# Kernel optimization log

Measured on AMD Instinct MI355X. Metric: run time of the kernel, lower is better.

The kernel has to match this reference:

```python
import jax, jax.numpy as jnp
import numpy as np

B, D, F, S, R = 2048, 1024, 1024, 64, 16


def _lora_dense(x, ids, kernel, bias, la, lb):
    # base: frozen dense path (stop_gradient mirrors the original module)
    base = x @ jax.lax.stop_gradient(kernel)
    if bias is not None:
        base = base + jax.lax.stop_gradient(bias)
    a = la[ids]            # (B, D, R) per-example adapter gather
    b = lb[ids]            # (B, R, F)
    low = jnp.einsum('bd,bdr->br', x, a)
    delta = jnp.einsum('br,brf->bf', low, b)
    return base + delta


def setup_inputs() -> dict:
    key = jax.random.key(0)
    ks = jax.random.split(key, 32)
    i = iter(range(32))
    d = {}
    d['carry'] = jax.random.normal(ks[next(i)], (B, F), jnp.float32)
    d['inputs'] = jax.random.normal(ks[next(i)], (B, D), jnp.float32)
    d['adapter_ids'] = jax.random.randint(ks[next(i)], (B,), 0, S)
    kscale = 1.0 / np.sqrt(D)
    for g in ['ir', 'iu', 'ic']:
        d[f'w_{g}'] = jax.random.normal(ks[next(i)], (D, F), jnp.float32) * kscale
        d[f'bias_{g}'] = jax.random.normal(ks[next(i)], (F,), jnp.float32) * 0.01
        d[f'la_{g}'] = jax.random.normal(ks[next(i)], (S, D, R), jnp.float32) * 0.02
        d[f'lb_{g}'] = jax.random.normal(ks[next(i)], (S, R, F), jnp.float32) * 0.01
    for g in ['rr', 'ru', 'rc']:
        d[f'w_{g}'] = jax.random.normal(ks[next(i)], (F, F), jnp.float32) * kscale
        d[f'la_{g}'] = jax.random.normal(ks[next(i)], (S, F, R), jnp.float32) * 0.02
        d[f'lb_{g}'] = jax.random.normal(ks[next(i)], (S, R, F), jnp.float32) * 0.01
    return d


def reference(carry, inputs, adapter_ids,
              w_ir, bias_ir, la_ir, lb_ir,
              w_iu, bias_iu, la_iu, lb_iu,
              w_ic, bias_ic, la_ic, lb_ic,
              w_rr, la_rr, lb_rr,
              w_ru, la_ru, lb_ru,
              w_rc, la_rc, lb_rc):
    ids = adapter_ids
    reset = jax.nn.sigmoid(
        _lora_dense(inputs, ids, w_ir, bias_ir, la_ir, lb_ir)
        + _lora_dense(carry, ids, w_rr, None, la_rr, lb_rr))
    update = jax.nn.sigmoid(
        _lora_dense(inputs, ids, w_iu, bias_iu, la_iu, lb_iu)
        + _lora_dense(carry, ids, w_ru, None, la_ru, lb_ru))
    candidate = jnp.tanh(
        _lora_dense(inputs, ids, w_ic, bias_ic, la_ic, lb_ic)
        + reset * _lora_dense(carry, ids, w_rc, None, la_rc, lb_rc))
    new_carry = (1.0 - update) * candidate + update * carry
    return new_carry
```

## Files before the change

### kernel.cpp

```cpp
#include <hip/hip_runtime.h>
#include <stdint.h>

#define B_  2048
#define D_  1024
#define F_  1024
#define S_  64
#define R_  16

typedef __attribute__((ext_vector_type(8))) short  s16x8;
typedef __attribute__((ext_vector_type(4))) unsigned short u16x4;
typedef __attribute__((ext_vector_type(8))) unsigned short u16x8;
typedef __attribute__((ext_vector_type(4))) float  f32x4;

__device__ __forceinline__ unsigned short f2b(float f){
  unsigned u = __float_as_uint(f);
  u = u + 0x7fffu + ((u >> 16) & 1u);
  return (unsigned short)(u >> 16);
}
__device__ __forceinline__ float b2f(unsigned short s){
  return __uint_as_float(((unsigned)s) << 16);
}

__device__ __forceinline__ void gload16(const void* g, void* l){
  __builtin_amdgcn_global_load_lds((const __attribute__((address_space(1))) unsigned int*)g,
                                   (__attribute__((address_space(3))) unsigned int*)l, 16, 0, 0);
}

#define W0OFF 0
#define W1OFF 2097152
#define W2OFF 4194304
#define W3OFF 5242880

__global__ __launch_bounds__(256) void prep_kernel(
    const float* __restrict__ x, const float* __restrict__ carry,
    unsigned short* __restrict__ XC,
    const float* __restrict__ w_ir, const float* __restrict__ w_rr,
    const float* __restrict__ w_iu, const float* __restrict__ w_ru,
    const float* __restrict__ w_ic, const float* __restrict__ w_rc,
    unsigned short* __restrict__ Wt_all,
    const int* __restrict__ ids, int* __restrict__ starts, int* __restrict__ order){
  int bx = blockIdx.x;
  int t = threadIdx.x;
  if (bx < 2048){
    int i = bx * 256 + t;
    int b = i >> 8;
    int j = (i & 255) * 4;
    float4 xv = *(const float4*)&x[(size_t)b*D_ + j];
    float4 cv = *(const float4*)&carry[(size_t)b*F_ + j];
    u16x4 xs, cs;
    xs[0]=f2b(xv.x); xs[1]=f2b(xv.y); xs[2]=f2b(xv.z); xs[3]=f2b(xv.w);
    cs[0]=f2b(cv.x); cs[1]=f2b(cv.y); cs[2]=f2b(cv.z); cs[3]=f2b(cv.w);
    *(u16x4*)&XC[(size_t)b*2048 + j]        = xs;
    *(u16x4*)&XC[(size_t)b*2048 + 1024 + j] = cs;
    return;
  }
  if (bx < 3584){
    int wb = bx - 2048;
    int g = wb >> 8, xb = wb & 255;
    const float* W; unsigned short* O; int st, ko;
    switch(g){
      case 0:  W=w_ir; O=Wt_all+W0OFF; st=2048; ko=0;    break;
      case 1:  W=w_rr; O=Wt_all+W0OFF; st=2048; ko=1024; break;
      case 2:  W=w_iu; O=Wt_all+W1OFF; st=2048; ko=0;    break;
      case 3:  W=w_ru; O=Wt_all+W1OFF; st=2048; ko=1024; break;
      case 4:  W=w_ic; O=Wt_all+W2OFF; st=1024; ko=0;    break;
      default: W=w_rc; O=Wt_all+W3OFF; st=1024; ko=0;    break;
    }
    __shared__ unsigned short T[64][72];
    int n0 = (xb & 15) * 64;
    int k0 = (xb >> 4) * 64;
    int c4 = (t & 15) * 4;
    int kk = t >> 4;
    #pragma unroll
    for (int i = 0; i < 4; i++){
      int k = kk + i*16;
      float4 v = *(const float4*)&W[(size_t)(k0+k)*F_ + n0 + c4];
      T[c4+0][k] = f2b(v.x); T[c4+1][k] = f2b(v.y); T[c4+2][k] = f2b(v.z); T[c4+3][k] = f2b(v.w);
    }
    __syncthreads();
    int n = t >> 2, ch = (t & 3) * 16;
    u16x8 a = *(const u16x8*)&T[n][ch];
    u16x8 b = *(const u16x8*)&T[n][ch+8];
    *(u16x8*)&O[(size_t)(n0+n)*st + ko + k0 + ch]     = a;
    *(u16x8*)&O[(size_t)(n0+n)*st + ko + k0 + ch + 8] = b;
    return;
  }
  __shared__ int cnt[S_]; __shared__ int off[S_+1]; __shared__ int cur[S_];
  if (t < S_) cnt[t] = 0;
  __syncthreads();
  for (int b = t; b < B_; b += 256) atomicAdd(&cnt[ids[b]], 1);
  __syncthreads();
  if (t == 0){ off[0] = 0; for (int s2 = 0; s2 < S_; s2++) off[s2+1] = off[s2] + cnt[s2]; }
  __syncthreads();
  if (t < S_) cur[t] = off[t];
  __syncthreads();
  for (int b = t; b < B_; b += 256){ int p = atomicAdd(&cur[ids[b]], 1); order[p] = b; }
  if (t < S_+1) starts[t] = off[t];
}

__global__ __launch_bounds__(256, 3) void gemm_low_kernel(
    const unsigned short* __restrict__ XC,
    const unsigned short* __restrict__ Wt_all,
    float* __restrict__ Yall,
    const float* __restrict__ la_ir, const float* __restrict__ la_iu,
    const float* __restrict__ la_ic, const float* __restrict__ la_rr,
    const float* __restrict__ la_ru, const float* __restrict__ la_rc,
    const int* __restrict__ starts, const int* __restrict__ order,
    float* __restrict__ low){
  __shared__ __align__(16) unsigned short smem[24576];
  int t = threadIdx.x;
  int bx = blockIdx.x;

  if (bx < 384){
    int s = bx & 63, g = bx / 64;
    const float* la;
    switch(g){ case 0: la=la_ir; break; case 1: la=la_iu; break; case 2: la=la_ic; break;
               case 3: la=la_rr; break; case 4: la=la_ru; break; default: la=la_rc; break; }
    int kofs = (g < 3) ? 0 : 1024;
    la += (size_t)s * D_ * R_;
    unsigned short* LA = smem;
    for (int i4 = t; i4 < D_*R_/4; i4 += 256){
      float4 v = *(const float4*)&la[i4*4];
      int d = i4 >> 2, r0 = (i4 & 3) * 4;
      LA[(r0+0)*1032 + d] = f2b(v.x);
      LA[(r0+1)*1032 + d] = f2b(v.y);
      LA[(r0+2)*1032 + d] = f2b(v.z);
      LA[(r0+3)*1032 + d] = f2b(v.w);
    }
    __syncthreads();
    int start = starts[s], cnt = starts[s+1] - start;
    if (cnt == 0) return;
    int lane = t & 63, wave = t >> 6;
    int l15 = lane & 15, kq = (lane >> 4) * 8;
    int ntiles = (cnt + 15) >> 4;
    for (int mt = wave*2; mt < ntiles; mt += 8){
      bool two = (mt + 1 < ntiles);
      int m0 = mt*16 + l15;       if (m0 >= cnt) m0 = cnt - 1;
      int m1 = (mt+1)*16 + l15;   if (m1 >= cnt) m1 = cnt - 1;
      int e0 = order[start + m0];
      int e1 = two ? order[start + m1] : e0;
      const unsigned short* A0 = XC + (size_t)e0*2048 + kofs + kq;
      const unsigned short* A1 = XC + (size_t)e1*2048 + kofs + kq;
      const unsigned short* Bp = &LA[l15*1032 + kq];
      f32x4 acc0 = {}, acc1 = {};
      #pragma unroll 4
      for (int kt = 0; kt < 1024; kt += 32){
        s16x8 a0 = *(const s16x8*)(A0 + kt);
        s16x8 a1 = *(const s16x8*)(A1 + kt);
        s16x8 b  = *(const s16x8*)(Bp + kt);
        acc0 = __builtin_amdgcn_mfma_f32_16x16x32_bf16(a0, b, acc0, 0, 0, 0);
        acc1 = __builtin_amdgcn_mfma_f32_16x16x32_bf16(a1, b, acc1, 0, 0, 0);
      }
      int rowb = (lane >> 4) * 4;
      #pragma unroll
      for (int i = 0; i < 4; i++){
        int m = mt*16 + rowb + i;
        if (m < cnt){
          int e = order[start + m];
          low[((size_t)g*B_ + e)*R_ + l15] = acc0[i];
        }
      }
      if (two){
        #pragma unroll
        for (int i = 0; i < 4; i++){
          int m = (mt+1)*16 + rowb + i;
          if (m < cnt){
            int e = order[start + m];
            low[((size_t)g*B_ + e)*R_ + l15] = acc1[i];
          }
        }
      }
    }
    return;
  }

  int bid = bx - 384;
  int u = bid >> 7;
  int tile = bid & 127;
  int K = (u < 2) ? 2048 : 1024;
  int kofs = (u == 3) ? 1024 : 0;
  const size_t uoffs[4] = {W0OFF, W1OFF, W2OFF, W3OFF};
  const unsigned short* Wt = Wt_all + uoffs[u];
  float* Y = Yall + (size_t)u * ((size_t)B_ * F_);

  unsigned short (*As)[4096] = (unsigned short(*)[4096])smem;
  unsigned short (*Bs)[4096] = (unsigned short(*)[4096])(smem + 12288);

  int lane = t & 63, wave = t >> 6;
  int mt = tile >> 3, nt = tile & 7;
  int row0 = mt * 128, col0 = nt * 128;
  int wrow = (wave >> 1) * 64, wcol = (wave & 1) * 64;

  int arow = t >> 2;
  int achk = ((t & 3) ^ ((t >> 3) & 3)) * 8;

  const unsigned short* Ab  = XC + (size_t)(row0 + arow) * 2048 + kofs + achk;
  const unsigned short* Ab2 = Ab + (size_t)64 * 2048;
  const unsigned short* Bb  = Wt + (size_t)(col0 + arow) * K + achk;
  const unsigned short* Bb2 = Bb + (size_t)64 * K;

  int l15 = lane & 15;
  int kof = (((lane >> 4) ^ ((l15 >> 1) & 3)) * 8);
  f32x4 acc[4][4] = {};

  gload16(Ab,      &As[0][t*8]);  gload16(Ab2,      &As[0][2048 + t*8]);
  gload16(Bb,      &Bs[0][t*8]);  gload16(Bb2,      &Bs[0][2048 + t*8]);
  gload16(Ab + 32, &As[1][t*8]);  gload16(Ab2 + 32, &As[1][2048 + t*8]);
  gload16(Bb + 32, &Bs[1][t*8]);  gload16(Bb2 + 32, &Bs[1][2048 + t*8]);

  int nsteps = K >> 5;
  int cur = 0;
  for (int tt = 0; tt < nsteps - 1; ++tt){
    asm volatile("s_waitcnt vmcnt(4)" ::: "memory");
    __builtin_amdgcn_s_barrier();
    asm volatile("" ::: "memory");
    s16x8 af[4], bfr[4];
    #pragma unroll
    for (int m = 0; m < 4; m++)
      af[m] = *(const s16x8*)&As[cur][(wrow + m*16 + l15)*32 + kof];
    #pragma unroll
    for (int n = 0; n < 4; n++)
      bfr[n] = *(const s16x8*)&Bs[cur][(wcol + n*16 + l15)*32 + kof];
    __builtin_amdgcn_s_setprio(1);
    #pragma unroll
    for (int m = 0; m < 4; m++){
      #pragma unroll
      for (int n = 0; n < 4; n++){
        acc[m][n] = __builtin_amdgcn_mfma_f32_16x16x32_bf16(af[m], bfr[n], acc[m][n], 0, 0, 0);
      }
    }
    __builtin_amdgcn_s_setprio(0);
    if (tt < nsteps - 2){
      int nb = cur + 2; if (nb >= 3) nb -= 3;
      int kt = (tt + 2) * 32;
      gload16(Ab  + kt, &As[nb][t*8]);  gload16(Ab2 + kt, &As[nb][2048 + t*8]);
      gload16(Bb  + kt, &Bs[nb][t*8]);  gload16(Bb2 + kt, &Bs[nb][2048 + t*8]);
    }
    cur = cur + 1; if (cur >= 3) cur -= 3;
  }
  asm volatile("s_waitcnt vmcnt(0)" ::: "memory");
  __builtin_amdgcn_s_barrier();
  asm volatile("" ::: "memory");
  {
    s16x8 af[4], bfr[4];
    #pragma unroll
    for (int m = 0; m < 4; m++)
      af[m] = *(const s16x8*)&As[cur][(wrow + m*16 + l15)*32 + kof];
    #pragma unroll
    for (int n = 0; n < 4; n++)
      bfr[n] = *(const s16x8*)&Bs[cur][(wcol + n*16 + l15)*32 + kof];
    #pragma unroll
    for (int m = 0; m < 4; m++){
      #pragma unroll
      for (int n = 0; n < 4; n++){
        acc[m][n] = __builtin_amdgcn_mfma_f32_16x16x32_bf16(af[m], bfr[n], acc[m][n], 0, 0, 0);
      }
    }
  }

  int orow = row0 + wrow + (lane >> 4) * 4;
  int ocol = col0 + wcol + l15;
  #pragma unroll
  for (int m = 0; m < 4; m++){
    #pragma unroll
    for (int n = 0; n < 4; n++){
      #pragma unroll
      for (int i = 0; i < 4; i++){
        Y[(size_t)(orow + m*16 + i) * F_ + ocol + n*16] = acc[m][n][i];
      }
    }
  }
}

__global__ __launch_bounds__(256) void delta_final_kernel(
    const float* __restrict__ carry,
    const float* __restrict__ bias_ir, const float* __restrict__ bias_iu,
    const float* __restrict__ bias_ic,
    const float* __restrict__ lb_ir, const float* __restrict__ lb_rr,
    const float* __restrict__ lb_iu, const float* __restrict__ lb_ru,
    const float* __restrict__ lb_ic, const float* __restrict__ lb_rc,
    const int* __restrict__ starts, const int* __restrict__ order,
    const float* __restrict__ low, const float* __restrict__ Yall,
    float* __restrict__ out){
  int s = blockIdx.x;
  int c0 = blockIdx.y * 128;
  __shared__ unsigned short Bsm[3 * 128 * 40];
  int t = threadIdx.x;
  const float* lbp[6] = {lb_ir, lb_rr, lb_iu, lb_ru, lb_ic, lb_rc};
  #pragma unroll
  for (int j = 0; j < 6; j++){
    const float* lb = lbp[j] + (size_t)s * R_ * F_;
    unsigned short* Bj = &Bsm[(j >> 1)*5120 + (j & 1)*16];
    #pragma unroll
    for (int it = 0; it < 2; it++){
      int idx = t + it*256;
      int r = idx >> 5, c4 = (idx & 31) * 4;
      float4 v = *(const float4*)&lb[(size_t)r*F_ + c0 + c4];
      Bj[(c4+0)*40 + r] = f2b(v.x);
      Bj[(c4+1)*40 + r] = f2b(v.y);
      Bj[(c4+2)*40 + r] = f2b(v.z);
      Bj[(c4+3)*40 + r] = f2b(v.w);
    }
  }
  __syncthreads();
  int start = starts[s], cnt = starts[s+1] - start;
  if (cnt == 0) return;
  int lane = t & 63, wave = t >> 6;
  int l15 = lane & 15, kq = (lane >> 4) * 8;
  int ntiles = (cnt + 15) >> 4;
  const float* Y0 = Yall + 0*(size_t)B_*F_;
  const float* Y1 = Yall + 1*(size_t)B_*F_;
  const float* Y2 = Yall + 2*(size_t)B_*F_;
  const float* Y3 = Yall + 3*(size_t)B_*F_;
  int k8 = kq & 15; bool hi = (kq >= 16);
  for (int pt = wave; pt < ntiles*2; pt += 4){
    int mt = pt >> 1, cf0 = (pt & 1) * 4;
    int m = mt*16 + l15; if (m >= cnt) m = cnt - 1;
    int e = order[start + m];
    s16x8 a_r, a_u, a_c1 = {}, a_c2 = {};
    {
      const float* p = &low[((size_t)(hi ? 3 : 0)*B_ + e)*R_ + k8];
      float4 v0 = *(const float4*)p, v1 = *(const float4*)(p+4);
      a_r[0]=f2b(v0.x); a_r[1]=f2b(v0.y); a_r[2]=f2b(v0.z); a_r[3]=f2b(v0.w);
      a_r[4]=f2b(v1.x); a_r[5]=f2b(v1.y); a_r[6]=f2b(v1.z); a_r[7]=f2b(v1.w);
    }
    {
      const float* p = &low[((size_t)(hi ? 4 : 1)*B_ + e)*R_ + k8];
      float4 v0 = *(const float4*)p, v1 = *(const float4*)(p+4);
      a_u[0]=f2b(v0.x); a_u[1]=f2b(v0.y); a_u[2]=f2b(v0.z); a_u[3]=f2b(v0.w);
      a_u[4]=f2b(v1.x); a_u[5]=f2b(v1.y); a_u[6]=f2b(v1.z); a_u[7]=f2b(v1.w);
    }
    if (!hi){
      const float* p = &low[((size_t)2*B_ + e)*R_ + k8];
      float4 v0 = *(const float4*)p, v1 = *(const float4*)(p+4);
      a_c1[0]=f2b(v0.x); a_c1[1]=f2b(v0.y); a_c1[2]=f2b(v0.z); a_c1[3]=f2b(v0.w);
      a_c1[4]=f2b(v1.x); a_c1[5]=f2b(v1.y); a_c1[6]=f2b(v1.z); a_c1[7]=f2b(v1.w);
    } else {
      const float* p = &low[((size_t)5*B_ + e)*R_ + k8];
      float4 v0 = *(const float4*)p, v1 = *(const float4*)(p+4);
      a_c2[0]=f2b(v0.x); a_c2[1]=f2b(v0.y); a_c2[2]=f2b(v0.z); a_c2[3]=f2b(v0.w);
      a_c2[4]=f2b(v1.x); a_c2[5]=f2b(v1.y); a_c2[6]=f2b(v1.z); a_c2[7]=f2b(v1.w);
    }
    int rowb = (lane >> 4) * 4;
    int erow[4]; bool wok[4];
    #pragma unroll
    for (int i = 0; i < 4; i++){
      int mm = mt*16 + rowb + i;
      wok[i] = (mm < cnt);
      erow[i] = order[start + (wok[i] ? mm : cnt - 1)];
    }
    #pragma unroll
    for (int cf = cf0; cf < cf0 + 4; cf++){
      int col = cf*16 + l15;
      s16x8 b_r = *(const s16x8*)&Bsm[0*5120 + col*40 + kq];
      s16x8 b_u = *(const s16x8*)&Bsm[1*5120 + col*40 + kq];
      s16x8 b_c = *(const s16x8*)&Bsm[2*5120 + col*40 + kq];
      f32x4 zero = {};
      f32x4 dr  = __builtin_amdgcn_mfma_f32_16x16x32_bf16(a_r,  b_r, zero, 0, 0, 0);
      f32x4 du  = __builtin_amdgcn_mfma_f32_16x16x32_bf16(a_u,  b_u, zero, 0, 0, 0);
      f32x4 dic = __builtin_amdgcn_mfma_f32_16x16x32_bf16(a_c1, b_c, zero, 0, 0, 0);
      f32x4 drc = __builtin_amdgcn_mfma_f32_16x16x32_bf16(a_c2, b_c, zero, 0, 0, 0);
      int oc = c0 + col;
      float br = bias_ir[oc], bu = bias_iu[oc], bc = bias_ic[oc];
      #pragma unroll
      for (int i = 0; i < 4; i++){
        if (wok[i]){
          size_t idx = (size_t)erow[i]*F_ + oc;
          float zr  = Y0[idx] + br + dr[i];
          float zu  = Y1[idx] + bu + du[i];
          float zic = Y2[idx] + bc + dic[i];
          float zrc = Y3[idx] + drc[i];
          float cv  = carry[idx];
          float rr = 1.f/(1.f+__expf(-zr));
          float uu = 1.f/(1.f+__expf(-zu));
          float a = zic + rr*zrc;
          float ee = __expf(-2.f*fabsf(a));
          float cand = copysignf((1.f-ee)/(1.f+ee), a);
          out[idx] = (1.f-uu)*cand + uu*cv;
        }
      }
    }
  }
}

extern "C" void kernel_launch(void* const* d_in, const int* in_sizes, int n_in,
                              void* d_out, int out_size, void* d_ws, size_t ws_size,
                              hipStream_t stream){
  const float* carry   = (const float*)d_in[0];
  const float* x       = (const float*)d_in[1];
  const int*   ids     = (const int*)d_in[2];
  const float* w_ir    = (const float*)d_in[3];
  const float* bias_ir = (const float*)d_in[4];
  const float* la_ir   = (const float*)d_in[5];
  const float* lb_ir   = (const float*)d_in[6];
  const float* w_iu    = (const float*)d_in[7];
  const float* bias_iu = (const float*)d_in[8];
  const float* la_iu   = (const float*)d_in[9];
  const float* lb_iu   = (const float*)d_in[10];
  const float* w_ic    = (const float*)d_in[11];
  const float* bias_ic = (const float*)d_in[12];
  const float* la_ic   = (const float*)d_in[13];
  const float* lb_ic   = (const float*)d_in[14];
  const float* w_rr    = (const float*)d_in[15];
  const float* la_rr   = (const float*)d_in[16];
  const float* lb_rr   = (const float*)d_in[17];
  const float* w_ru    = (const float*)d_in[18];
  const float* la_ru   = (const float*)d_in[19];
  const float* lb_ru   = (const float*)d_in[20];
  const float* w_rc    = (const float*)d_in[21];
  const float* la_rc   = (const float*)d_in[22];
  const float* lb_rc   = (const float*)d_in[23];

  char* ws = (char*)d_ws;
  unsigned short* XC     = (unsigned short*)(ws + 0);
  unsigned short* Wt_all = (unsigned short*)(ws + 8388608);
  float* Yall = (float*)(ws + 20971520);
  float* low  = (float*)(ws + 54525952);
  int* starts = (int*)(ws + 55312384);
  int* order  = (int*)(ws + 55313408);

  prep_kernel<<<dim3(3585), dim3(256), 0, stream>>>(x, carry, XC,
                                                    w_ir, w_rr, w_iu, w_ru, w_ic, w_rc,
                                                    Wt_all, ids, starts, order);
  gemm_low_kernel<<<dim3(896), dim3(256), 0, stream>>>(XC, Wt_all, Yall,
                                                       la_ir, la_iu, la_ic,
                                                       la_rr, la_ru, la_rc,
                                                       starts, order, low);
  delta_final_kernel<<<dim3(64, 8), dim3(256), 0, stream>>>(carry, bias_ir, bias_iu, bias_ic,
                                                            lb_ir, lb_rr, lb_iu, lb_ru,
                                                            lb_ic, lb_rc,
                                                            starts, order, low, Yall,
                                                            (float*)d_out);
}
```

Baseline: 90.90 us.

## Use 256x128 GEMM tiles, double buffering, and bf16 intermediate outputs

The base GEMM tile grows from 128x128 to 256x128, so each wave computes a 128x64 sub-tile with 8x4 MFMA accumulators. The 3-stage pipeline built on vmcnt waits is replaced by a 2-buffer scheme with full __syncthreads, and the GEMM blocks move ahead of the LoRA low-rank blocks in the grid. The intermediate Y results are stored as bf16 instead of fp32, halving that write and read traffic between kernels. The cost is more register pressure (launch bounds drop to 2 blocks per CU), fewer GEMM blocks (256 instead of 512) for parallelism, a weaker load/compute overlap, and extra rounding error in the pre-activation values.

New measurement: 90.28 us. Within noise of the previous version (-0.7%).

```diff
diff --git a/kernel.cpp b/kernel.cpp
--- a/kernel.cpp
+++ b/kernel.cpp
@@ -98,10 +98,10 @@
   if (t < S_+1) starts[t] = off[t];
 }
 
-__global__ __launch_bounds__(256, 3) void gemm_low_kernel(
+__global__ __launch_bounds__(256, 2) void gemm_low_kernel(
     const unsigned short* __restrict__ XC,
     const unsigned short* __restrict__ Wt_all,
-    float* __restrict__ Yall,
+    unsigned short* __restrict__ Yall,
     const float* __restrict__ la_ir, const float* __restrict__ la_iu,
     const float* __restrict__ la_ic, const float* __restrict__ la_rr,
     const float* __restrict__ la_ru, const float* __restrict__ la_rc,
@@ -111,8 +111,9 @@
   int t = threadIdx.x;
   int bx = blockIdx.x;
 
-  if (bx < 384){
-    int s = bx & 63, g = bx / 64;
+  if (bx >= 256){
+    int lb = bx - 256;
+    int s = lb & 63, g = lb >> 6;
     const float* la;
     switch(g){ case 0: la=la_ir; break; case 1: la=la_iu; break; case 2: la=la_ic; break;
                case 3: la=la_rr; break; case 4: la=la_ru; break; default: la=la_rc; break; }
@@ -174,99 +175,94 @@
     return;
   }
 
-  int bid = bx - 384;
-  int u = bid >> 7;
-  int tile = bid & 127;
+  int u = bx >> 6;
+  int tile = bx & 63;
   int K = (u < 2) ? 2048 : 1024;
   int kofs = (u == 3) ? 1024 : 0;
   const size_t uoffs[4] = {W0OFF, W1OFF, W2OFF, W3OFF};
   const unsigned short* Wt = Wt_all + uoffs[u];
-  float* Y = Yall + (size_t)u * ((size_t)B_ * F_);
-
-  unsigned short (*As)[4096] = (unsigned short(*)[4096])smem;
-  unsigned short (*Bs)[4096] = (unsigned short(*)[4096])(smem + 12288);
+  unsigned short* Y = Yall + (size_t)u * ((size_t)B_ * F_);
+
+  unsigned short (*As)[8192] = (unsigned short(*)[8192])smem;
+  unsigned short (*Bs)[4096] = (unsigned short(*)[4096])(smem + 16384);
 
   int lane = t & 63, wave = t >> 6;
   int mt = tile >> 3, nt = tile & 7;
-  int row0 = mt * 128, col0 = nt * 128;
-  int wrow = (wave >> 1) * 64, wcol = (wave & 1) * 64;
+  int row0 = mt * 256, col0 = nt * 128;
+  int wrow = (wave >> 1) * 128, wcol = (wave & 1) * 64;
 
   int arow = t >> 2;
   int achk = ((t & 3) ^ ((t >> 3) & 3)) * 8;
 
-  const unsigned short* Ab  = XC + (size_t)(row0 + arow) * 2048 + kofs + achk;
-  const unsigned short* Ab2 = Ab + (size_t)64 * 2048;
-  const unsigned short* Bb  = Wt + (size_t)(col0 + arow) * K + achk;
-  const unsigned short* Bb2 = Bb + (size_t)64 * K;
+  const unsigned short* Ab = XC + (size_t)(row0 + arow) * 2048 + kofs + achk;
+  const unsigned short* Bb = Wt + (size_t)(col0 + arow) * K + achk;
 
   int l15 = lane & 15;
   int kof = (((lane >> 4) ^ ((l15 >> 1) & 3)) * 8);
-  f32x4 acc[4][4] = {};
-
-  gload16(Ab,      &As[0][t*8]);  gload16(Ab2,      &As[0][2048 + t*8]);
-  gload16(Bb,      &Bs[0][t*8]);  gload16(Bb2,      &Bs[0][2048 + t*8]);
-  gload16(Ab + 32, &As[1][t*8]);  gload16(Ab2 + 32, &As[1][2048 + t*8]);
-  gload16(Bb + 32, &Bs[1][t*8]);  gload16(Bb2 + 32, &Bs[1][2048 + t*8]);
+  f32x4 acc[8][4] = {};
+
+#define STAGE_T(bf, kt) \
+  gload16(Ab + (kt),                       &As[bf][t*8]);        \
+  gload16(Ab + (size_t)64*2048 + (kt),     &As[bf][2048 + t*8]); \
+  gload16(Ab + (size_t)128*2048 + (kt),    &As[bf][4096 + t*8]); \
+  gload16(Ab + (size_t)192*2048 + (kt),    &As[bf][6144 + t*8]); \
+  gload16(Bb + (kt),                       &Bs[bf][t*8]);        \
+  gload16(Bb + (size_t)64*K + (kt),        &Bs[bf][2048 + t*8]);
+
+  STAGE_T(0, 0);
+  __syncthreads();
 
   int nsteps = K >> 5;
   int cur = 0;
   for (int tt = 0; tt < nsteps - 1; ++tt){
-    asm volatile("s_waitcnt vmcnt(4)" ::: "memory");
-    __builtin_amdgcn_s_barrier();
-    asm volatile("" ::: "memory");
-    s16x8 af[4], bfr[4];
-    #pragma unroll
-    for (int m = 0; m < 4; m++)
+    int nxt = cur ^ 1;
+    STAGE_T(nxt, (tt + 1) * 32);
+    s16x8 af[8], bfr[4];
+    #pragma unroll
+    for (int m = 0; m < 8; m++)
       af[m] = *(const s16x8*)&As[cur][(wrow + m*16 + l15)*32 + kof];
     #pragma unroll
     for (int n = 0; n < 4; n++)
       bfr[n] = *(const s16x8*)&Bs[cur][(wcol + n*16 + l15)*32 + kof];
     __builtin_amdgcn_s_setprio(1);
     #pragma unroll
-    for (int m = 0; m < 4; m++){
+    for (int m = 0; m < 8; m++){
       #pragma unroll
       for (int n = 0; n < 4; n++){
         acc[m][n] = __builtin_amdgcn_mfma_f32_16x16x32_bf16(af[m], bfr[n], acc[m][n], 0, 0, 0);
       }
     }
     __builtin_amdgcn_s_setprio(0);
-    if (tt < nsteps - 2){
-      int nb = cur + 2; if (nb >= 3) nb -= 3;
-      int kt = (tt + 2) * 32;
-      gload16(Ab  + kt, &As[nb][t*8]);  gload16(Ab2 + kt, &As[nb][2048 + t*8]);
-      gload16(Bb  + kt, &Bs[nb][t*8]);  gload16(Bb2 + kt, &Bs[nb][2048 + t*8]);
-    }
-    cur = cur + 1; if (cur >= 3) cur -= 3;
-  }
-  asm volatile("s_waitcnt vmcnt(0)" ::: "memory");
-  __builtin_amdgcn_s_barrier();
-  asm volatile("" ::: "memory");
+    __syncthreads();
+    cur = nxt;
+  }
   {
-    s16x8 af[4], bfr[4];
-    #pragma unroll
-    for (int m = 0; m < 4; m++)
+    s16x8 af[8], bfr[4];
+    #pragma unroll
+    for (int m = 0; m < 8; m++)
       af[m] = *(const s16x8*)&As[cur][(wrow + m*16 + l15)*32 + kof];
     #pragma unroll
     for (int n = 0; n < 4; n++)
       bfr[n] = *(const s16x8*)&Bs[cur][(wcol + n*16 + l15)*32 + kof];
     #pragma unroll
-    for (int m = 0; m < 4; m++){
+    for (int m = 0; m < 8; m++){
       #pragma unroll
       for (int n = 0; n < 4; n++){
         acc[m][n] = __builtin_amdgcn_mfma_f32_16x16x32_bf16(af[m], bfr[n], acc[m][n], 0, 0, 0);
       }
     }
   }
+#undef STAGE_T
 
   int orow = row0 + wrow + (lane >> 4) * 4;
   int ocol = col0 + wcol + l15;
   #pragma unroll
-  for (int m = 0; m < 4; m++){
+  for (int m = 0; m < 8; m++){
     #pragma unroll
     for (int n = 0; n < 4; n++){
       #pragma unroll
       for (int i = 0; i < 4; i++){
-        Y[(size_t)(orow + m*16 + i) * F_ + ocol + n*16] = acc[m][n][i];
+        Y[(size_t)(orow + m*16 + i) * F_ + ocol + n*16] = f2b(acc[m][n][i]);
       }
     }
   }
@@ -280,7 +276,7 @@
     const float* __restrict__ lb_iu, const float* __restrict__ lb_ru,
     const float* __restrict__ lb_ic, const float* __restrict__ lb_rc,
     const int* __restrict__ starts, const int* __restrict__ order,
-    const float* __restrict__ low, const float* __restrict__ Yall,
+    const float* __restrict__ low, const unsigned short* __restrict__ Yall,
     float* __restrict__ out){
   int s = blockIdx.x;
   int c0 = blockIdx.y * 128;
@@ -308,10 +304,10 @@
   int lane = t & 63, wave = t >> 6;
   int l15 = lane & 15, kq = (lane >> 4) * 8;
   int ntiles = (cnt + 15) >> 4;
-  const float* Y0 = Yall + 0*(size_t)B_*F_;
-  const float* Y1 = Yall + 1*(size_t)B_*F_;
-  const float* Y2 = Yall + 2*(size_t)B_*F_;
-  const float* Y3 = Yall + 3*(size_t)B_*F_;
+  const unsigned short* Y0 = Yall + 0*(size_t)B_*F_;
+  const unsigned short* Y1 = Yall + 1*(size_t)B_*F_;
+  const unsigned short* Y2 = Yall + 2*(size_t)B_*F_;
+  const unsigned short* Y3 = Yall + 3*(size_t)B_*F_;
   int k8 = kq & 15; bool hi = (kq >= 16);
   for (int pt = wave; pt < ntiles*2; pt += 4){
     int mt = pt >> 1, cf0 = (pt & 1) * 4;
@@ -366,10 +362,10 @@
       for (int i = 0; i < 4; i++){
         if (wok[i]){
           size_t idx = (size_t)erow[i]*F_ + oc;
-          float zr  = Y0[idx] + br + dr[i];
-          float zu  = Y1[idx] + bu + du[i];
-          float zic = Y2[idx] + bc + dic[i];
-          float zrc = Y3[idx] + drc[i];
+          float zr  = b2f(Y0[idx]) + br + dr[i];
+          float zu  = b2f(Y1[idx]) + bu + du[i];
+          float zic = b2f(Y2[idx]) + bc + dic[i];
+          float zrc = b2f(Y3[idx]) + drc[i];
           float cv  = carry[idx];
           float rr = 1.f/(1.f+__expf(-zr));
           float uu = 1.f/(1.f+__expf(-zu));
@@ -414,15 +410,15 @@
   char* ws = (char*)d_ws;
   unsigned short* XC     = (unsigned short*)(ws + 0);
   unsigned short* Wt_all = (unsigned short*)(ws + 8388608);
-  float* Yall = (float*)(ws + 20971520);
-  float* low  = (float*)(ws + 54525952);
-  int* starts = (int*)(ws + 55312384);
-  int* order  = (int*)(ws + 55313408);
+  unsigned short* Yall   = (unsigned short*)(ws + 20971520);
+  float* low  = (float*)(ws + 37748736);
+  int* starts = (int*)(ws + 38535168);
+  int* order  = (int*)(ws + 38536192);
 
   prep_kernel<<<dim3(3585), dim3(256), 0, stream>>>(x, carry, XC,
                                                     w_ir, w_rr, w_iu, w_ru, w_ic, w_rc,
                                                     Wt_all, ids, starts, order);
-  gemm_low_kernel<<<dim3(896), dim3(256), 0, stream>>>(XC, Wt_all, Yall,
+  gemm_low_kernel<<<dim3(640), dim3(256), 0, stream>>>(XC, Wt_all, Yall,
                                                        la_ir, la_iu, la_ic,
                                                        la_rr, la_ru, la_rc,
                                                        starts, order, low);
```
